# Optimization experiments

Hardware: AMD Instinct MI355X
Metric: run time of the kernel (lower is better)

Reference implementation:

```python
import jax, jax.numpy as jnp
import numpy as np

N_CLASS = 5      # episode way
SHOTS = 5        # support images per class
D = 64           # local descriptor dim (feature_dim)
H = W = 16       # feature map spatial size
N_QUERY = 75     # 15 queries per class


def setup_inputs() -> dict:
    key = jax.random.key(0)
    k1, k2 = jax.random.split(key)
    support = jax.random.normal(k1, (N_CLASS * SHOTS, D, H, W), dtype=jnp.float32)
    query = jax.random.normal(k2, (N_QUERY, D, H, W), dtype=jnp.float32)
    return {"support": support, "query": query, "task_index": 0, "k": 3, "k2": 64}


def reference(support, query, task_index, k, k2):
    C = N_CLASS
    n, d, h, w = support.shape
    hw = h * w
    ns = n // C  # shots per class

    # Per-class support descriptors: [C, ns*h*w, d], L2-normalized along d
    s = support.reshape(C, ns, d, hw)
    s = jnp.transpose(s, (0, 1, 3, 2)).reshape(C, ns * hw, d)
    s = s / jnp.linalg.norm(s, axis=-1, keepdims=True)

    # Query local descriptors: [B, d, Nq], L2-normalized along d
    B = query.shape[0]
    q = query.reshape(B, d, -1)
    q = q / jnp.linalg.norm(q, axis=1, keepdims=True)

    # Cosine similarity per class: [C, B, Nq, M]  (M = ns*h*w support descriptors)
    sim = jnp.einsum('cmd,bdq->cbqm', s, q)

    # torch.topk(sim, k, dim=1): top-k over support descriptors M per query location
    v = jax.lax.top_k(sim, k)[0]          # [C, B, Nq, k]
    v = jnp.swapaxes(v, 2, 3)             # [C, B, k, Nq]
    # torch.topk(., k2, dim=2): top-k2 over query locations
    v = jax.lax.top_k(v, k2)[0]           # [C, B, k, k2]

    # cat over classes, unsqueeze, then view(-1, 1, k, k2)
    return v.reshape(-1, 1, k, k2)        # [C*B, 1, k, k2]
```

## Files before the change

### kernel.cpp

```cpp
#include <hip/hip_runtime.h>
#include <stdint.h>


#define C_CLS 5
#define SHOTS 5
#define DIM 64
#define HW 256
#define NQ 75
#define K1 3
#define K2 64
#define M_TOT 1280
#define MQ 4
#define MQROWS (M_TOT / MQ)
#define TROWS 64
#define NIT (MQROWS / TROWS)
#define QG 2

using bf16x8 = __attribute__((ext_vector_type(8))) short;
using f32x4  = __attribute__((ext_vector_type(4))) float;

typedef __attribute__((address_space(1))) const unsigned int GU32;
typedef __attribute__((address_space(3))) unsigned int LU32;

__device__ __forceinline__ void gload16(const void* g, void* l) {
    __builtin_amdgcn_global_load_lds((GU32*)g, (LU32*)l, 16, 0, 0);
}

#define SWZ(o) ((o) ^ ((((o) >> 7) & 7) << 4))

__device__ inline unsigned short f2bf(float x) {
    uint32_t u = __float_as_uint(x);
    u += 0x7FFF + ((u >> 16) & 1);
    return (unsigned short)(u >> 16);
}

__device__ __forceinline__ void ins3(float v, float& t0, float& t1, float& t2) {
    t2 = __builtin_amdgcn_fmed3f(v, t1, t2);
    t1 = __builtin_amdgcn_fmed3f(v, t0, t1);
    t0 = fmaxf(t0, v);
}

__global__ __launch_bounds__(256)
void prep(const float* __restrict__ support, const float* __restrict__ query,
          unsigned short* __restrict__ Sn, unsigned short* __restrict__ Qn) {
    const int tid  = threadIdx.x;
    const int wv   = tid >> 6, lane = tid & 63;
    const int dg   = lane >> 4, dl = lane & 15;
    const int bid  = blockIdx.x;
    const float* src;
    unsigned short* dst;
    if (bid < NQ * 4) {
        const int b    = bid >> 2;
        const int desc = (bid & 3) * 64 + wv * 16 + dl;
        src = query + (size_t)b * DIM * HW + desc;
        dst = Qn + ((size_t)b * HW + desc) * DIM + dg * 16;
    } else {
        const int sb   = bid - NQ * 4;
        const int cs   = sb >> 2;
        const int desc = (sb & 3) * 64 + wv * 16 + dl;
        const int c = cs / SHOTS, s = cs % SHOTS;
        src = support + (size_t)cs * DIM * HW + desc;
        dst = Sn + ((size_t)c * M_TOT + s * HW + desc) * DIM + dg * 16;
    }
    float v[16];
    float nrm = 0.f;
#pragma unroll
    for (int i = 0; i < 16; ++i) {
        const float x = src[(dg * 16 + i) * HW];
        v[i] = x; nrm = fmaf(x, x, nrm);
    }
    nrm += __shfl_xor(nrm, 16, 64);
    nrm += __shfl_xor(nrm, 32, 64);
    const float inv = rsqrtf(nrm);
    uint32_t p[8];
#pragma unroll
    for (int j = 0; j < 8; ++j)
        p[j] = (uint32_t)f2bf(v[2 * j] * inv) | ((uint32_t)f2bf(v[2 * j + 1] * inv) << 16);
    const uint4 w0 = {p[0], p[1], p[2], p[3]}, w1 = {p[4], p[5], p[6], p[7]};
    ((uint4*)dst)[0] = w0;
    ((uint4*)dst)[1] = w1;
}

__global__ __launch_bounds__(512)
void dn4_mfma(const unsigned short* __restrict__ Sn,
              const unsigned short* __restrict__ Qn,
              unsigned short* __restrict__ partial) {
    __shared__ unsigned short sB[2][TROWS * DIM];

    const int tid  = threadIdx.x;
    const int lane = tid & 63, w = tid >> 6;
    const int c15  = lane & 15, kg = lane >> 4;
    const int bid  = blockIdx.x;
    const int b    = bid % NQ;
    const int cq   = bid / NQ;
    const int c    = cq >> 2, qt = cq & 3;

    bf16x8 aq[QG][2];
    const int q0 = b * HW + w * (QG * 16);
#pragma unroll
    for (int g = 0; g < QG; ++g) {
        const unsigned short* qp = Qn + (size_t)(q0 + g * 16 + c15) * DIM + kg * 8;
        aq[g][0] = *(const bf16x8*)qp;
        aq[g][1] = *(const bf16x8*)(qp + 32);
    }

    float t0[QG][4], t1[QG][4], t2[QG][4];
#pragma unroll
    for (int g = 0; g < QG; ++g)
#pragma unroll
        for (int r = 0; r < 4; ++r) { t0[g][r] = -2.f; t1[g][r] = -2.f; t2[g][r] = -2.f; }

    const int sw   = (c15 & 7) << 4;
    const int off0 = (kg * 16) ^ sw;
    const int off1 = (kg * 16 + 64) ^ sw;
    const int rowb = c15 * 128;

    const char* tb0 = (const char*)(Sn + ((size_t)c * M_TOT + qt * MQROWS) * DIM);

    gload16(tb0 + SWZ(tid * 16), (char*)sB[0] + w * 1024);
    __syncthreads();

    int cur = 0;
    for (int it = 0; it < NIT; ++it) {
        if (it < NIT - 1) {
            const char* tb = tb0 + (size_t)(it + 1) * (TROWS * DIM * 2);
            gload16(tb + SWZ(tid * 16), (char*)sB[cur ^ 1] + w * 1024);
        }
#pragma unroll
        for (int ns = 0; ns < 4; ++ns) {
            const char* rp = (const char*)sB[cur] + rowb + ns * 2048;
            const bf16x8 b0 = *(const bf16x8*)(rp + off0);
            const bf16x8 b1 = *(const bf16x8*)(rp + off1);
#pragma unroll
            for (int g = 0; g < QG; ++g) {
                f32x4 acc = {0.f, 0.f, 0.f, 0.f};
                acc = __builtin_amdgcn_mfma_f32_16x16x32_bf16(aq[g][0], b0, acc, 0, 0, 0);
                acc = __builtin_amdgcn_mfma_f32_16x16x32_bf16(aq[g][1], b1, acc, 0, 0, 0);
#pragma unroll
                for (int r = 0; r < 4; ++r)
                    ins3(acc[r], t0[g][r], t1[g][r], t2[g][r]);
            }
        }
        __syncthreads();
        cur ^= 1;
    }

#pragma unroll
    for (int g = 0; g < QG; ++g)
#pragma unroll
        for (int r = 0; r < 4; ++r)
#pragma unroll
            for (int off = 1; off < 16; off <<= 1) {
                const float o0 = __shfl_xor(t0[g][r], off, 64);
                const float o1 = __shfl_xor(t1[g][r], off, 64);
                const float o2 = __shfl_xor(t2[g][r], off, 64);
                ins3(o0, t0[g][r], t1[g][r], t2[g][r]);
                ins3(o1, t0[g][r], t1[g][r], t2[g][r]);
                ins3(o2, t0[g][r], t1[g][r], t2[g][r]);
            }

    if (c15 == 0) {
        unsigned short* pbase =
            partial + (((size_t)(c * NQ + b) * MQ + qt) * K1) * HW;
#pragma unroll
        for (int g = 0; g < QG; ++g)
#pragma unroll
            for (int r = 0; r < 4; ++r) {
                const int qloc = w * (QG * 16) + g * 16 + kg * 4 + r;
                pbase[qloc]          = f2bf(t0[g][r]);
                pbase[HW + qloc]     = f2bf(t1[g][r]);
                pbase[2 * HW + qloc] = f2bf(t2[g][r]);
            }
    }
}

__global__ __launch_bounds__(256)
void dn4_topq(const unsigned short* __restrict__ partial, float* __restrict__ out) {
    __shared__ float sbuf[HW];
    const int tid = threadIdx.x;
    const int bid = blockIdx.x;
    const int ki  = bid % K1;
    const int cb  = bid / K1;

    const unsigned short* p = partial + (size_t)cb * MQ * K1 * HW + tid;
    float t0 = -2.f, t1 = -2.f, t2 = -2.f;
#pragma unroll
    for (int h = 0; h < MQ; ++h)
#pragma unroll
        for (int r = 0; r < K1; ++r) {
            const float v = __uint_as_float((uint32_t)p[(h * K1 + r) * HW] << 16);
            ins3(v, t0, t1, t2);
        }
    float v = (ki == 0) ? t0 : (ki == 1) ? t1 : t2;

#pragma unroll
    for (int kk = 2; kk <= HW; kk <<= 1) {
#pragma unroll
        for (int j = kk >> 1; j > 0; j >>= 1) {
            const bool keep_max = (((tid & kk) == 0) == ((tid & j) == 0));
            float wv;
            if (j >= 64) {
                sbuf[tid] = v;
                __syncthreads();
                wv = sbuf[tid ^ j];
                __syncthreads();
            } else {
                wv = __shfl_xor(v, j, 64);
            }
            v = keep_max ? fmaxf(v, wv) : fminf(v, wv);
        }
    }
    if (tid < K2) out[(size_t)cb * K1 * K2 + (size_t)ki * K2 + tid] = v;
}

extern "C" void kernel_launch(void* const* d_in, const int* in_sizes, int n_in,
                              void* d_out, int out_size, void* d_ws, size_t ws_size,
                              hipStream_t stream) {
    const float* support = (const float*)d_in[0];
    const float* query   = (const float*)d_in[1];
    float* out = (float*)d_out;

    char* ws = (char*)d_ws;
    unsigned short* Sn      = (unsigned short*)ws;
    unsigned short* Qn      = (unsigned short*)(ws + 819200);
    unsigned short* partial = (unsigned short*)(ws + 819200 + 2457600);

    prep    <<<dim3(400),               dim3(256), 0, stream>>>(support, query, Sn, Qn);
    dn4_mfma<<<dim3(C_CLS * MQ * NQ),   dim3(512), 0, stream>>>(Sn, Qn, partial);
    dn4_topq<<<dim3(C_CLS * NQ * K1),   dim3(256), 0, stream>>>(partial, out);
}
```

Before: 51.06 us.

## Store normalized descriptors in MFMA fragment order and split support into halves

The prep kernel now writes normalized bf16 descriptors directly in the per-lane MFMA operand layout. The main kernel can then load A and B fragments with contiguous 16-byte reads, with no LDS swizzling or strided row loads. The support set is split into 2 halves of 640 rows, loaded in 128-row tiles, instead of 4 quarters of 64-row tiles. This halves the block count and the partial results to merge, and the partials are now stored as fp32 instead of bf16. Fewer, larger blocks may reduce parallelism, and the fp32 partials double the write size per entry.

```diff
diff --git a/kernel.cpp b/kernel.cpp
--- a/kernel.cpp
+++ b/kernel.cpp
@@ -10,13 +10,13 @@
 #define K1 3
 #define K2 64
 #define M_TOT 1280
-#define MQ 4
-#define MQROWS (M_TOT / MQ)
-#define TROWS 64
-#define NIT (MQROWS / TROWS)
+#define MHALF 640
+#define TROWS 128
+#define NIT (MHALF / TROWS)
 #define QG 2
 
 using bf16x8 = __attribute__((ext_vector_type(8))) short;
+using u32x4  = __attribute__((ext_vector_type(4))) unsigned int;
 using f32x4  = __attribute__((ext_vector_type(4))) float;
 
 typedef __attribute__((address_space(1))) const unsigned int GU32;
@@ -25,8 +25,6 @@
 __device__ __forceinline__ void gload16(const void* g, void* l) {
     __builtin_amdgcn_global_load_lds((GU32*)g, (LU32*)l, 16, 0, 0);
 }
-
-#define SWZ(o) ((o) ^ ((((o) >> 7) & 7) << 4))
 
 __device__ inline unsigned short f2bf(float x) {
     uint32_t u = __float_as_uint(x);
@@ -48,19 +46,19 @@
     const int dg   = lane >> 4, dl = lane & 15;
     const int bid  = blockIdx.x;
     const float* src;
-    unsigned short* dst;
+    unsigned short* dstblk;
     if (bid < NQ * 4) {
         const int b    = bid >> 2;
         const int desc = (bid & 3) * 64 + wv * 16 + dl;
-        src = query + (size_t)b * DIM * HW + desc;
-        dst = Qn + ((size_t)b * HW + desc) * DIM + dg * 16;
+        src    = query + (size_t)b * DIM * HW + desc;
+        dstblk = Qn + (size_t)b * 16384 + (size_t)((bid & 3) * 4 + wv) * 1024;
     } else {
         const int sb   = bid - NQ * 4;
         const int cs   = sb >> 2;
         const int desc = (sb & 3) * 64 + wv * 16 + dl;
         const int c = cs / SHOTS, s = cs % SHOTS;
-        src = support + (size_t)cs * DIM * HW + desc;
-        dst = Sn + ((size_t)c * M_TOT + s * HW + desc) * DIM + dg * 16;
+        src    = support + (size_t)cs * DIM * HW + desc;
+        dstblk = Sn + (size_t)c * 81920 + (size_t)(s * 16 + (sb & 3) * 4 + wv) * 1024;
     }
     float v[16];
     float nrm = 0.f;
@@ -76,33 +74,37 @@
 #pragma unroll
     for (int j = 0; j < 8; ++j)
         p[j] = (uint32_t)f2bf(v[2 * j] * inv) | ((uint32_t)f2bf(v[2 * j + 1] * inv) << 16);
-    const uint4 w0 = {p[0], p[1], p[2], p[3]}, w1 = {p[4], p[5], p[6], p[7]};
-    ((uint4*)dst)[0] = w0;
-    ((uint4*)dst)[1] = w1;
+    const int ck = dg >> 1;
+#pragma unroll
+    for (int q = 0; q < 2; ++q) {
+        const int kg = (dg & 1) * 2 + q;
+        uint4 wq = {p[q * 4 + 0], p[q * 4 + 1], p[q * 4 + 2], p[q * 4 + 3]};
+        *(uint4*)(dstblk + ck * 512 + (kg * 16 + dl) * 8) = wq;
+    }
 }
 
 __global__ __launch_bounds__(512)
 void dn4_mfma(const unsigned short* __restrict__ Sn,
               const unsigned short* __restrict__ Qn,
-              unsigned short* __restrict__ partial) {
+              float* __restrict__ partial) {
     __shared__ unsigned short sB[2][TROWS * DIM];
 
     const int tid  = threadIdx.x;
     const int lane = tid & 63, w = tid >> 6;
     const int c15  = lane & 15, kg = lane >> 4;
     const int bid  = blockIdx.x;
-    const int b    = bid % NQ;
-    const int cq   = bid / NQ;
-    const int c    = cq >> 2, qt = cq & 3;
+    const int half = bid & 1;
+    const int cb   = bid >> 1;
+    const int c    = cb / NQ, b = cb % NQ;
 
     bf16x8 aq[QG][2];
-    const int q0 = b * HW + w * (QG * 16);
-#pragma unroll
-    for (int g = 0; g < QG; ++g) {
-        const unsigned short* qp = Qn + (size_t)(q0 + g * 16 + c15) * DIM + kg * 8;
-        aq[g][0] = *(const bf16x8*)qp;
-        aq[g][1] = *(const bf16x8*)(qp + 32);
-    }
+    const unsigned short* qf = Qn + (size_t)b * 16384 + (size_t)(w * 2) * 1024;
+#pragma unroll
+    for (int g = 0; g < QG; ++g)
+#pragma unroll
+        for (int ck = 0; ck < 2; ++ck)
+            aq[g][ck] = __builtin_bit_cast(bf16x8,
+                *(const u32x4*)(qf + g * 1024 + ck * 512 + lane * 8));
 
     float t0[QG][4], t1[QG][4], t2[QG][4];
 #pragma unroll
@@ -110,31 +112,31 @@
 #pragma unroll
         for (int r = 0; r < 4; ++r) { t0[g][r] = -2.f; t1[g][r] = -2.f; t2[g][r] = -2.f; }
 
-    const int sw   = (c15 & 7) << 4;
-    const int off0 = (kg * 16) ^ sw;
-    const int off1 = (kg * 16 + 64) ^ sw;
-    const int rowb = c15 * 128;
-
-    const char* tb0 = (const char*)(Sn + ((size_t)c * M_TOT + qt * MQROWS) * DIM);
-
-    gload16(tb0 + SWZ(tid * 16), (char*)sB[0] + w * 1024);
+    const f32x4 Z = {0.f, 0.f, 0.f, 0.f};
+    const char* tb0 = (const char*)(Sn + (size_t)c * 81920 + (size_t)half * 40960);
+
+#pragma unroll
+    for (int rep = 0; rep < 2; ++rep)
+        gload16(tb0 + rep * 8192 + tid * 16, (char*)sB[0] + rep * 8192 + w * 1024);
     __syncthreads();
 
     int cur = 0;
     for (int it = 0; it < NIT; ++it) {
         if (it < NIT - 1) {
-            const char* tb = tb0 + (size_t)(it + 1) * (TROWS * DIM * 2);
-            gload16(tb + SWZ(tid * 16), (char*)sB[cur ^ 1] + w * 1024);
+            const char* tb = tb0 + (size_t)(it + 1) * 16384;
+#pragma unroll
+            for (int rep = 0; rep < 2; ++rep)
+                gload16(tb + rep * 8192 + tid * 16,
+                        (char*)sB[cur ^ 1] + rep * 8192 + w * 1024);
         }
 #pragma unroll
-        for (int ns = 0; ns < 4; ++ns) {
-            const char* rp = (const char*)sB[cur] + rowb + ns * 2048;
-            const bf16x8 b0 = *(const bf16x8*)(rp + off0);
-            const bf16x8 b1 = *(const bf16x8*)(rp + off1);
+        for (int ns = 0; ns < 8; ++ns) {
+            const unsigned short* rp = &sB[cur][ns * 1024 + lane * 8];
+            const bf16x8 b0 = __builtin_bit_cast(bf16x8, *(const u32x4*)rp);
+            const bf16x8 b1 = __builtin_bit_cast(bf16x8, *(const u32x4*)(rp + 512));
 #pragma unroll
             for (int g = 0; g < QG; ++g) {
-                f32x4 acc = {0.f, 0.f, 0.f, 0.f};
-                acc = __builtin_amdgcn_mfma_f32_16x16x32_bf16(aq[g][0], b0, acc, 0, 0, 0);
+                f32x4 acc = __builtin_amdgcn_mfma_f32_16x16x32_bf16(aq[g][0], b0, Z, 0, 0, 0);
                 acc = __builtin_amdgcn_mfma_f32_16x16x32_bf16(aq[g][1], b1, acc, 0, 0, 0);
 #pragma unroll
                 for (int r = 0; r < 4; ++r)
@@ -160,37 +162,34 @@
             }
 
     if (c15 == 0) {
-        unsigned short* pbase =
-            partial + (((size_t)(c * NQ + b) * MQ + qt) * K1) * HW;
+        float* pbase = partial + ((size_t)(cb * 2 + half) * K1) * HW;
 #pragma unroll
         for (int g = 0; g < QG; ++g)
 #pragma unroll
             for (int r = 0; r < 4; ++r) {
-                const int qloc = w * (QG * 16) + g * 16 + kg * 4 + r;
-                pbase[qloc]          = f2bf(t0[g][r]);
-                pbase[HW + qloc]     = f2bf(t1[g][r]);
-                pbase[2 * HW + qloc] = f2bf(t2[g][r]);
+                const int qloc = (w * 2 + g) * 16 + kg * 4 + r;
+                pbase[qloc]          = t0[g][r];
+                pbase[HW + qloc]     = t1[g][r];
+                pbase[2 * HW + qloc] = t2[g][r];
             }
     }
 }
 
 __global__ __launch_bounds__(256)
-void dn4_topq(const unsigned short* __restrict__ partial, float* __restrict__ out) {
+void dn4_topq(const float* __restrict__ partial, float* __restrict__ out) {
     __shared__ float sbuf[HW];
     const int tid = threadIdx.x;
     const int bid = blockIdx.x;
     const int ki  = bid % K1;
     const int cb  = bid / K1;
 
-    const unsigned short* p = partial + (size_t)cb * MQ * K1 * HW + tid;
+    const float* p = partial + (size_t)cb * 2 * K1 * HW + tid;
     float t0 = -2.f, t1 = -2.f, t2 = -2.f;
 #pragma unroll
-    for (int h = 0; h < MQ; ++h)
-#pragma unroll
-        for (int r = 0; r < K1; ++r) {
-            const float v = __uint_as_float((uint32_t)p[(h * K1 + r) * HW] << 16);
-            ins3(v, t0, t1, t2);
-        }
+    for (int h = 0; h < 2; ++h)
+#pragma unroll
+        for (int r = 0; r < K1; ++r)
+            ins3(p[(h * K1 + r) * HW], t0, t1, t2);
     float v = (ki == 0) ? t0 : (ki == 1) ? t1 : t2;
 
 #pragma unroll
@@ -221,11 +220,11 @@
     float* out = (float*)d_out;
 
     char* ws = (char*)d_ws;
-    unsigned short* Sn      = (unsigned short*)ws;
-    unsigned short* Qn      = (unsigned short*)(ws + 819200);
-    unsigned short* partial = (unsigned short*)(ws + 819200 + 2457600);
-
-    prep    <<<dim3(400),               dim3(256), 0, stream>>>(support, query, Sn, Qn);
-    dn4_mfma<<<dim3(C_CLS * MQ * NQ),   dim3(512), 0, stream>>>(Sn, Qn, partial);
-    dn4_topq<<<dim3(C_CLS * NQ * K1),   dim3(256), 0, stream>>>(partial, out);
-}
+    unsigned short* Sn = (unsigned short*)ws;
+    unsigned short* Qn = (unsigned short*)(ws + 819200);
+    float* partial     = (float*)(ws + 819200 + 2457600);
+
+    prep    <<<dim3(400),              dim3(256), 0, stream>>>(support, query, Sn, Qn);
+    dn4_mfma<<<dim3(C_CLS * NQ * 2),   dim3(512), 0, stream>>>(Sn, Qn, partial);
+    dn4_topq<<<dim3(C_CLS * NQ * K1),  dim3(256), 0, stream>>>(partial, out);
+}
```

After: 51.87 us. Within noise of the previous version (+1.6%).
